# Optimization experiments

Measured on AMD Instinct MI355X. Metric: run time of the kernel, lower is better.

The kernel has to match this reference:

```python
import jax, jax.numpy as jnp
import numpy as np

N = 50000          # nodes
E = 800000         # edges
IN_C = 128
HID = 64
NUM_GRAPHS = 256
OUT_C = 8


def setup_inputs() -> dict:
    key = jax.random.key(0)
    k1, k2, k3, k4, k5, k6, k7 = jax.random.split(key, 7)
    x = jax.random.normal(k1, (N, IN_C), dtype=jnp.float32)
    edge_index = jax.random.randint(k2, (2, E), 0, N, dtype=jnp.int64)
    batch = jnp.sort(jax.random.randint(k3, (N,), 0, NUM_GRAPHS, dtype=jnp.int64))
    # GCNConv params (lin: in->hid, glorot-ish) and fc params (hid->8)
    W = jax.random.normal(k4, (IN_C, HID), dtype=jnp.float32) / np.sqrt(IN_C)
    b = jnp.zeros((HID,), dtype=jnp.float32)
    Wfc = jax.random.normal(k5, (HID, OUT_C), dtype=jnp.float32) / np.sqrt(HID)
    bfc = jnp.zeros((OUT_C,), dtype=jnp.float32)
    return {"x": x, "edge_index": edge_index, "batch": batch,
            "W": W, "b": b, "Wfc": Wfc, "bfc": bfc}


def reference(x, edge_index, batch, W, b, Wfc, bfc):
    n = x.shape[0]
    # GCNConv: linear transform first, then normalized propagation w/ self-loops
    x_lin = x @ W                                             # [N, HID]
    self_loops = jnp.arange(n, dtype=edge_index.dtype)
    row = jnp.concatenate([edge_index[0], self_loops])        # src
    col = jnp.concatenate([edge_index[1], self_loops])        # dst
    # symmetric normalization: deg over destinations (weight = 1)
    deg = jax.ops.segment_sum(jnp.ones_like(col, dtype=x.dtype), col,
                              num_segments=n)                 # [N]
    dinv = jnp.where(deg > 0, jax.lax.rsqrt(deg), 0.0)
    norm = dinv[row] * dinv[col]                              # [E+N]
    msg = x_lin[row] * norm[:, None]                          # gather + scale
    h = jax.ops.segment_sum(msg, col, num_segments=n) + b     # scatter-add
    h = jax.nn.relu(h)
    # global_mean_pool over batch ids
    sums = jax.ops.segment_sum(h, batch, num_segments=NUM_GRAPHS)
    cnts = jax.ops.segment_sum(jnp.ones((n,), dtype=x.dtype), batch,
                               num_segments=NUM_GRAPHS)
    pooled = sums / jnp.maximum(cnts, 1.0)[:, None]           # [G, HID]
    return pooled @ Wfc + bfc                                 # [G, 8]
```

## Files before the change

### kernel.cpp

```cpp
#include <hip/hip_runtime.h>
#include <stdint.h>

#define N_NODES 50000
#define N_EDGES 800000
#define IN_C    128
#define HID     64
#define NUM_G   256
#define OUT_C   8

#define NBH   64
#define ES    (N_EDGES / NBH)
#define NBIN  50048
#define NPK   (NBIN / 2)

#define NQ_H   4
#define BINS_H (NBIN / NQ_H)
#define PK_H   (BINS_H / 2)
#define NQ_S   8
#define BINS_S (NBIN / NQ_S)

#define NBLK_CSR   98
#define NBLK_LIN   512
#define NTILE      1563
#define NBLK_SCALE 200
#define NCHUNK     (N_NODES * 8)

__device__ __forceinline__ unsigned short f2bf(float f) {
    union { float f; unsigned u; } v; v.f = f;
    unsigned r = v.u + 0x7fff + ((v.u >> 16) & 1);
    return (unsigned short)(r >> 16);
}
__device__ __forceinline__ float4 bf4(uint2 u) {
    union { unsigned u; float f; } a, b, c, d;
    a.u = u.x << 16;  b.u = u.x & 0xffff0000u;
    c.u = u.y << 16;  d.u = u.y & 0xffff0000u;
    return make_float4(a.f, b.f, c.f, d.f);
}

__global__ __launch_bounds__(256) void k_histB(const int* __restrict__ col,
                                               int* __restrict__ part,
                                               int* __restrict__ cnt) {
    __shared__ int lh[PK_H];
    const int tid = threadIdx.x;
    if (blockIdx.x == 0 && tid == 0)
        __hip_atomic_store(&cnt[0], 0, __ATOMIC_RELAXED, __HIP_MEMORY_SCOPE_AGENT);
    const int r = blockIdx.x >> 2;
    const int q = blockIdx.x & 3;
    const int q0 = q * BINS_H;
    for (int i = tid; i < PK_H; i += 256) lh[i] = 0;
    __syncthreads();
    const int4* col4 = (const int4*)(col + r * ES);
#pragma unroll 2
    for (int j4 = tid; j4 < ES / 4; j4 += 256) {
        int4 c = col4[j4];
        unsigned d0 = (unsigned)(c.x - q0), d1 = (unsigned)(c.y - q0);
        unsigned d2 = (unsigned)(c.z - q0), d3 = (unsigned)(c.w - q0);
        if (d0 < BINS_H) atomicAdd(&lh[d0 >> 1], 1 << ((d0 & 1) * 16));
        if (d1 < BINS_H) atomicAdd(&lh[d1 >> 1], 1 << ((d1 & 1) * 16));
        if (d2 < BINS_H) atomicAdd(&lh[d2 >> 1], 1 << ((d2 & 1) * 16));
        if (d3 < BINS_H) atomicAdd(&lh[d3 >> 1], 1 << ((d3 & 1) * 16));
    }
    __syncthreads();
    int* dst = part + r * NPK + q * PK_H;
    for (int i = tid; i < PK_H; i += 256) dst[i] = lh[i];
}

__global__ __launch_bounds__(256, 3) void k_csrlin(
        int* __restrict__ part, float* __restrict__ dinv,
        int* __restrict__ nstart, const int* __restrict__ batch,
        int* __restrict__ gstart, float* __restrict__ pooled,
        int* __restrict__ agg, int* __restrict__ cnt,
        const float* __restrict__ x, const float* __restrict__ W,
        float* __restrict__ y) {
    __shared__ int smemI[12512];
    const int tid = threadIdx.x;
    const int b   = blockIdx.x;

    if (b >= NBLK_CSR) {
        float* xs = (float*)smemI;
        float* Ws = (float*)smemI + 4224;
        {
            const float4* wsrc = (const float4*)W;
            float4*       wdst = (float4*)Ws;
#pragma unroll
            for (int j = 0; j < 8; ++j) wdst[tid + 256 * j] = wsrc[tid + 256 * j];
        }
        const int ty = tid >> 4, tx = tid & 15;
        const int r0 = ty * 2, c0 = tx * 4;
        for (int tile = b - NBLK_CSR; tile < NTILE; tile += NBLK_LIN) {
            const int row0 = tile * 32;
            __syncthreads();
            {
                const float4* src = (const float4*)(x + (size_t)row0 * IN_C);
                for (int i4 = tid; i4 < 1024; i4 += 256) {
                    int r = i4 >> 5, c4 = i4 & 31;
                    float4 v = make_float4(0.f, 0.f, 0.f, 0.f);
                    if (row0 + r < N_NODES) v = src[i4];
                    *(float4*)&xs[r * 132 + c4 * 4] = v;
                }
            }
            __syncthreads();
            float acc[2][4] = {};
#define FMA4(a_, bv_, r_) { acc[r_][0]=fmaf(a_,bv_.x,acc[r_][0]); acc[r_][1]=fmaf(a_,bv_.y,acc[r_][1]); \
                            acc[r_][2]=fmaf(a_,bv_.z,acc[r_][2]); acc[r_][3]=fmaf(a_,bv_.w,acc[r_][3]); }
            for (int k = 0; k < IN_C; k += 4) {
                float4 a0 = *(float4*)&xs[(r0 + 0) * 132 + k];
                float4 a1 = *(float4*)&xs[(r0 + 1) * 132 + k];
                float4 b0 = *(const float4*)&Ws[(k + 0) * HID + c0];
                float4 b1 = *(const float4*)&Ws[(k + 1) * HID + c0];
                float4 b2 = *(const float4*)&Ws[(k + 2) * HID + c0];
                float4 b3 = *(const float4*)&Ws[(k + 3) * HID + c0];
                FMA4(a0.x, b0, 0) FMA4(a0.y, b1, 0) FMA4(a0.z, b2, 0) FMA4(a0.w, b3, 0)
                FMA4(a1.x, b0, 1) FMA4(a1.y, b1, 1) FMA4(a1.z, b2, 1) FMA4(a1.w, b3, 1)
            }
#undef FMA4
#pragma unroll
            for (int i = 0; i < 2; ++i) {
                int r = row0 + r0 + i;
                if (r < N_NODES)
                    *(float4*)&y[(size_t)r * HID + c0] =
                        make_float4(acc[i][0], acc[i][1], acc[i][2], acc[i][3]);
            }
        }
        return;
    }

    int* sScan   = smemI;
    int* sAgg    = smemI + 256;
    int* sPrefix = smemI + 256 + 128;
    const int t = b * 256 + tid;
    const bool valid = t < NPK;
    int s0 = 0, s1 = 0;
    if (valid) {
        int idx = t;
#pragma unroll 4
        for (int r = 0; r < NBH; ++r, idx += NPK) {
            int v = part[idx];
            part[idx] = s0 | (s1 << 16);
            s0 += v & 0xffff;
            s1 += (v >> 16) & 0xffff;
        }
        ((float2*)dinv)[t] = make_float2(rsqrtf((float)(s0 + 1)),
                                         rsqrtf((float)(s1 + 1)));
    }
    int ps = s0 + s1;
    sScan[tid] = ps;
    __syncthreads();
    int acc = ps;
#pragma unroll
    for (int off = 1; off < 256; off <<= 1) {
        int tv = (tid >= off) ? sScan[tid - off] : 0;
        __syncthreads();
        acc += tv;
        sScan[tid] = acc;
        __syncthreads();
    }
    const int excl  = acc - ps;
    const int total = sScan[255];
    if (tid == 0) {
        __hip_atomic_store(&agg[b], total, __ATOMIC_RELAXED, __HIP_MEMORY_SCOPE_AGENT);
        __hip_atomic_fetch_add(&cnt[0], 1, __ATOMIC_RELEASE, __HIP_MEMORY_SCOPE_AGENT);
        while (__hip_atomic_load(&cnt[0], __ATOMIC_ACQUIRE, __HIP_MEMORY_SCOPE_AGENT) < NBLK_CSR)
            __builtin_amdgcn_s_sleep(2);
    }
    __syncthreads();
    if (tid < NBLK_CSR)
        sAgg[tid] = __hip_atomic_load(&agg[tid], __ATOMIC_RELAXED, __HIP_MEMORY_SCOPE_AGENT);
    __syncthreads();
    if (tid == 0) {
        int p = 0;
        for (int j = 0; j < b; ++j) p += sAgg[j];
        sPrefix[0] = p;
    }
    __syncthreads();
    if (valid) {
        int base = sPrefix[0] + excl;
        ((int2*)nstart)[t] = make_int2(base, base + s0);
    }
    if (t <= NUM_G) {
        int lo = 0, hi = N_NODES;
        while (lo < hi) {
            int mid = (lo + hi) >> 1;
            if (batch[mid] < t) lo = mid + 1; else hi = mid;
        }
        gstart[t] = lo;
    }
    if (t < NUM_G * HID) pooled[t] = 0.f;
}

__global__ __launch_bounds__(256) void k_scatscale(
        const int* __restrict__ row, const int* __restrict__ col,
        const int* __restrict__ part, const int* __restrict__ nstart,
        int* __restrict__ ed,
        const float* __restrict__ y, const float* __restrict__ dinv,
        unsigned short* __restrict__ yb) {
    const int tid = threadIdx.x;
    if (blockIdx.x >= NQ_S * NBH) {
        int idx = (blockIdx.x - NQ_S * NBH) * 256 + tid;
#pragma unroll 1
        for (int c = idx; c < NCHUNK; c += NBLK_SCALE * 256) {
            int r  = c >> 3, ch = c & 7;
            const float4* ysrc = (const float4*)(y + (size_t)r * HID + ch * 8);
            float4 a = ysrc[0], b = ysrc[1];
            float dv = dinv[r];
            uint4 o;
            o.x = (unsigned)f2bf(a.x * dv) | ((unsigned)f2bf(a.y * dv) << 16);
            o.y = (unsigned)f2bf(a.z * dv) | ((unsigned)f2bf(a.w * dv) << 16);
            o.z = (unsigned)f2bf(b.x * dv) | ((unsigned)f2bf(b.y * dv) << 16);
            o.w = (unsigned)f2bf(b.z * dv) | ((unsigned)f2bf(b.w * dv) << 16);
            *(uint4*)&yb[(size_t)r * HID + ch * 8] = o;
        }
        return;
    }
    __shared__ int lc[BINS_S];
    const int r = blockIdx.x >> 3;
    const int q = blockIdx.x & 7;
    const int q0 = q * BINS_S;
    for (int i = tid; i < BINS_S; i += 256) {
        int bin = q0 + i;
        int bb  = part[r * NPK + (bin >> 1)];
        int off = (i & 1) ? ((bb >> 16) & 0xffff) : (bb & 0xffff);
        lc[i] = nstart[bin] + off;
    }
    __syncthreads();
    const int4* col4 = (const int4*)(col + r * ES);
    const int4* row4 = (const int4*)(row + r * ES);
#pragma unroll 2
    for (int j4 = tid; j4 < ES / 4; j4 += 256) {
        int4 c = col4[j4];
        int4 s = row4[j4];
        unsigned d0 = (unsigned)(c.x - q0), d1 = (unsigned)(c.y - q0);
        unsigned d2 = (unsigned)(c.z - q0), d3 = (unsigned)(c.w - q0);
        if (d0 < BINS_S) ed[atomicAdd(&lc[d0], 1)] = s.x;
        if (d1 < BINS_S) ed[atomicAdd(&lc[d1], 1)] = s.y;
        if (d2 < BINS_S) ed[atomicAdd(&lc[d2], 1)] = s.z;
        if (d3 < BINS_S) ed[atomicAdd(&lc[d3], 1)] = s.w;
    }
}

#define GNPT 4
__global__ __launch_bounds__(256) void k_gpool(const int* __restrict__ ed,
                                               const int* __restrict__ nstart,
                                               const float* __restrict__ dinv,
                                               const unsigned short* __restrict__ yb,
                                               const int* __restrict__ batch,
                                               const float* __restrict__ bias,
                                               float* __restrict__ pooled) {
    __shared__ float spool[4 * HID];
    __shared__ int   sg0;
    const int tid  = threadIdx.x;
    const int lane = tid & 63;
    const int grp  = lane >> 4;
    const int sl   = lane & 15;
    const int nb0  = blockIdx.x * 64;

    for (int i = tid; i < 4 * HID; i += 256) spool[i] = 0.f;
    if (tid == 0) sg0 = batch[nb0];
    __syncthreads();
    const int sg0v = sg0;

    const int base = nb0 + (tid >> 6) * 16 + grp * GNPT;
    if (base < N_NODES) {
        const float4 b4 = *(const float4*)&bias[4 * sl];

#define FLUSH(g_, v_) { int slot_ = (g_) - sg0v; \
        if (slot_ < 4) { \
            atomicAdd(&spool[slot_ * HID + 4 * sl + 0], v_.x); \
            atomicAdd(&spool[slot_ * HID + 4 * sl + 1], v_.y); \
            atomicAdd(&spool[slot_ * HID + 4 * sl + 2], v_.z); \
            atomicAdd(&spool[slot_ * HID + 4 * sl + 3], v_.w); \
        } else { \
            atomicAdd(&pooled[(g_) * HID + 4 * sl + 0], v_.x); \
            atomicAdd(&pooled[(g_) * HID + 4 * sl + 1], v_.y); \
            atomicAdd(&pooled[(g_) * HID + 4 * sl + 2], v_.z); \
            atomicAdd(&pooled[(g_) * HID + 4 * sl + 3], v_.w); \
        } }

        int bnd[GNPT + 1];
#pragma unroll
        for (int i = 0; i <= GNPT; ++i) bnd[i] = nstart[base + i];
        int bt[GNPT];
#pragma unroll
        for (int i = 0; i < GNPT; ++i) bt[i] = batch[base + i];
        float dvv[GNPT];
#pragma unroll
        for (int i = 0; i < GNPT; ++i) dvv[i] = dinv[base + i];

        float4 pacc = make_float4(0.f, 0.f, 0.f, 0.f);
        int    cur  = -1;
#pragma unroll
        for (int n = 0; n < GNPT; ++n) {
            const int node = base + n;
            const int n0 = bnd[n], n1 = bnd[n + 1];
            float4 fa = make_float4(0.f, 0.f, 0.f, 0.f);
            float4 fb = make_float4(0.f, 0.f, 0.f, 0.f);
            int t = n0;
#pragma unroll 1
            for (; t + 4 <= n1; t += 4) {
                int s0 = ed[t], s1 = ed[t + 1], s2 = ed[t + 2], s3 = ed[t + 3];
                uint2 u0 = *(const uint2*)&yb[(size_t)s0 * HID + 4 * sl];
                uint2 u1 = *(const uint2*)&yb[(size_t)s1 * HID + 4 * sl];
                uint2 u2 = *(const uint2*)&yb[(size_t)s2 * HID + 4 * sl];
                uint2 u3 = *(const uint2*)&yb[(size_t)s3 * HID + 4 * sl];
                float4 v0 = bf4(u0), v1 = bf4(u1), v2 = bf4(u2), v3 = bf4(u3);
                fa.x += v0.x + v2.x;  fb.x += v1.x + v3.x;
                fa.y += v0.y + v2.y;  fb.y += v1.y + v3.y;
                fa.z += v0.z + v2.z;  fb.z += v1.z + v3.z;
                fa.w += v0.w + v2.w;  fb.w += v1.w + v3.w;
            }
#pragma unroll 1
            for (; t < n1; ++t) {
                int s = ed[t];
                uint2 u = *(const uint2*)&yb[(size_t)s * HID + 4 * sl];
                float4 v = bf4(u);
                fa.x += v.x; fa.y += v.y; fa.z += v.z; fa.w += v.w;
            }
            uint2 us = *(const uint2*)&yb[(size_t)node * HID + 4 * sl];
            float4 vs = bf4(us);
            float dv = dvv[n];
            float4 hv;
            hv.x = fmaxf((fa.x + fb.x + vs.x) * dv + b4.x, 0.f);
            hv.y = fmaxf((fa.y + fb.y + vs.y) * dv + b4.y, 0.f);
            hv.z = fmaxf((fa.z + fb.z + vs.z) * dv + b4.z, 0.f);
            hv.w = fmaxf((fa.w + fb.w + vs.w) * dv + b4.w, 0.f);
            int bg = bt[n];
            if (bg != cur) {
                if (cur >= 0) FLUSH(cur, pacc)
                cur  = bg;
                pacc = hv;
            } else {
                pacc.x += hv.x; pacc.y += hv.y; pacc.z += hv.z; pacc.w += hv.w;
            }
        }
        if (cur >= 0) FLUSH(cur, pacc)
#undef FLUSH
    }
    __syncthreads();
    for (int i = tid; i < 4 * HID; i += 256) {
        float v = spool[i];
        int g = sg0v + (i >> 6);
        if (v != 0.f && g < NUM_G)
            atomicAdd(&pooled[g * HID + (i & 63)], v);
    }
}

__global__ void k_out(const float* __restrict__ pooled, const int* __restrict__ gstart,
                      const float* __restrict__ Wfc, const float* __restrict__ bfc,
                      float* __restrict__ out) {
    int idx = blockIdx.x * blockDim.x + threadIdx.x;
    int g = idx >> 3;
    int o = idx & 7;
    float inv = 1.f / fmaxf((float)(gstart[g + 1] - gstart[g]), 1.f);
    float acc = 0.f;
#pragma unroll
    for (int k = 0; k < HID; ++k) acc += pooled[g * HID + k] * Wfc[k * OUT_C + o];
    out[idx] = acc * inv + bfc[o];
}

extern "C" void kernel_launch(void* const* d_in, const int* in_sizes, int n_in,
                              void* d_out, int out_size, void* d_ws, size_t ws_size,
                              hipStream_t stream) {
    const float* x     = (const float*)d_in[0];
    const int*   eidx  = (const int*)d_in[1];
    const int*   batch = (const int*)d_in[2];
    const float* W     = (const float*)d_in[3];
    const float* b     = (const float*)d_in[4];
    const float* Wfc   = (const float*)d_in[5];
    const float* bfc   = (const float*)d_in[6];
    float*       out   = (float*)d_out;

    const int* row = eidx;
    const int* col = eidx + N_EDGES;

    char* p = (char*)d_ws;
    float*          y    = (float*)p;          p += (size_t)N_NODES * HID * 4;
    unsigned short* yb   = (unsigned short*)p; p += (size_t)N_NODES * HID * 2;
    int*   part   = (int*)p;    p += (size_t)NBH * NPK * 4;
    float* dinv   = (float*)p;  p += (size_t)NBIN * 4;
    float* pooled = (float*)p;  p += (size_t)NUM_G * HID * 4;
    int*   nstart = (int*)p;    p += (size_t)(NBIN + 8) * 4;
    int*   gstart = (int*)p;    p += 1040;
    int*   agg    = (int*)p;    p += 512;
    int*   cnt    = (int*)p;    p += 64;
    int*   ed     = (int*)p;

    k_histB    <<<NBH * NQ_H, 256, 0, stream>>>(col, part, cnt);
    k_csrlin   <<<NBLK_CSR + NBLK_LIN, 256, 0, stream>>>(part, dinv, nstart, batch,
                                                         gstart, pooled, agg, cnt,
                                                         x, W, y);
    k_scatscale<<<NQ_S * NBH + NBLK_SCALE, 256, 0, stream>>>(row, col, part, nstart,
                                                             ed, y, dinv, yb);
    k_gpool    <<<(N_NODES + 63) / 64, 256, 0, stream>>>(ed, nstart, dinv, yb, batch,
                                                         b, pooled);
    k_out      <<<8, 256, 0, stream>>>(pooled, gstart, Wfc, bfc, out);
}
```

Measured before the change: 88.94 us.

## Fuse final FC into gpool via last-block counter and halve nodes per thread

Removes the separate k_out launch by having the last finishing k_gpool block, detected through an atomic counter in cnt[1], compute the pooled-mean FC output. It also halves nodes per thread group (GNPT 4→2) and doubles the gpool grid so more blocks share the gather work. In exchange it adds a per-block global atomic and relies on acquire/release ordering so the last block sees all pooled atomics. Smaller blocks also send more flushes to the shared-memory and global pooled accumulators.

```diff
diff --git a/kernel.cpp b/kernel.cpp
--- a/kernel.cpp
+++ b/kernel.cpp
@@ -24,6 +24,7 @@
 #define NTILE      1563
 #define NBLK_SCALE 200
 #define NCHUNK     (N_NODES * 8)
+#define GPOOL_GRID 1563
 
 __device__ __forceinline__ unsigned short f2bf(float f) {
     union { float f; unsigned u; } v; v.f = f;
@@ -42,8 +43,8 @@
                                                int* __restrict__ cnt) {
     __shared__ int lh[PK_H];
     const int tid = threadIdx.x;
-    if (blockIdx.x == 0 && tid == 0)
-        __hip_atomic_store(&cnt[0], 0, __ATOMIC_RELAXED, __HIP_MEMORY_SCOPE_AGENT);
+    if (blockIdx.x == 0 && tid < 2)
+        __hip_atomic_store(&cnt[tid], 0, __ATOMIC_RELAXED, __HIP_MEMORY_SCOPE_AGENT);
     const int r = blockIdx.x >> 2;
     const int q = blockIdx.x & 3;
     const int q0 = q * BINS_H;
@@ -238,28 +239,33 @@
     }
 }
 
-#define GNPT 4
+#define GNPT 2
 __global__ __launch_bounds__(256) void k_gpool(const int* __restrict__ ed,
                                                const int* __restrict__ nstart,
                                                const float* __restrict__ dinv,
                                                const unsigned short* __restrict__ yb,
                                                const int* __restrict__ batch,
                                                const float* __restrict__ bias,
-                                               float* __restrict__ pooled) {
+                                               float* __restrict__ pooled,
+                                               const int* __restrict__ gstart,
+                                               const float* __restrict__ Wfc,
+                                               const float* __restrict__ bfc,
+                                               float* __restrict__ out,
+                                               int* __restrict__ cnt) {
     __shared__ float spool[4 * HID];
     __shared__ int   sg0;
     const int tid  = threadIdx.x;
     const int lane = tid & 63;
     const int grp  = lane >> 4;
     const int sl   = lane & 15;
-    const int nb0  = blockIdx.x * 64;
+    const int nb0  = blockIdx.x * 32;
 
     for (int i = tid; i < 4 * HID; i += 256) spool[i] = 0.f;
     if (tid == 0) sg0 = batch[nb0];
     __syncthreads();
     const int sg0v = sg0;
 
-    const int base = nb0 + (tid >> 6) * 16 + grp * GNPT;
+    const int base = nb0 + (tid >> 6) * 8 + grp * GNPT;
     if (base < N_NODES) {
         const float4 b4 = *(const float4*)&bias[4 * sl];
 
@@ -342,19 +348,28 @@
         if (v != 0.f && g < NUM_G)
             atomicAdd(&pooled[g * HID + (i & 63)], v);
     }
-}
-
-__global__ void k_out(const float* __restrict__ pooled, const int* __restrict__ gstart,
-                      const float* __restrict__ Wfc, const float* __restrict__ bfc,
-                      float* __restrict__ out) {
-    int idx = blockIdx.x * blockDim.x + threadIdx.x;
-    int g = idx >> 3;
-    int o = idx & 7;
-    float inv = 1.f / fmaxf((float)(gstart[g + 1] - gstart[g]), 1.f);
-    float acc = 0.f;
-#pragma unroll
-    for (int k = 0; k < HID; ++k) acc += pooled[g * HID + k] * Wfc[k * OUT_C + o];
-    out[idx] = acc * inv + bfc[o];
+    __shared__ int lastFlag;
+    __syncthreads();
+    if (tid == 0) {
+        int prev = __hip_atomic_fetch_add(&cnt[1], 1, __ATOMIC_ACQ_REL, __HIP_MEMORY_SCOPE_AGENT);
+        lastFlag = (prev == GPOOL_GRID - 1) ? 1 : 0;
+    }
+    __syncthreads();
+    if (lastFlag) {
+        int g = tid;
+        int g0 = gstart[g], g1 = gstart[g + 1];
+        float inv = 1.f / fmaxf((float)(g1 - g0), 1.f);
+        float acc[OUT_C] = {};
+        for (int k = 0; k < HID; ++k) {
+            float pv = pooled[g * HID + k];
+#pragma unroll
+            for (int o = 0; o < OUT_C; ++o)
+                acc[o] = fmaf(pv, Wfc[k * OUT_C + o], acc[o]);
+        }
+#pragma unroll
+        for (int o = 0; o < OUT_C; ++o)
+            out[g * OUT_C + o] = acc[o] * inv + bfc[o];
+    }
 }
 
 extern "C" void kernel_launch(void* const* d_in, const int* in_sizes, int n_in,
@@ -390,7 +405,6 @@
                                                          x, W, y);
     k_scatscale<<<NQ_S * NBH + NBLK_SCALE, 256, 0, stream>>>(row, col, part, nstart,
                                                              ed, y, dinv, yb);
-    k_gpool    <<<(N_NODES + 63) / 64, 256, 0, stream>>>(ed, nstart, dinv, yb, batch,
-                                                         b, pooled);
-    k_out      <<<8, 256, 0, stream>>>(pooled, gstart, Wfc, bfc, out);
-}
+    k_gpool    <<<GPOOL_GRID, 256, 0, stream>>>(ed, nstart, dinv, yb, batch, b,
+                                                pooled, gstart, Wfc, bfc, out, cnt);
+}
```

After: 108.2 us. +21.6%, slower.
